# Performance work log

Measured on AMD Instinct MI355X. Metric: run time of the kernel, lower is better.

Reference implementation:

```python
import jax, jax.numpy as jnp
import numpy as np
import math

B, N, D, H = 4, 1024, 256, 8  # batch, points, dim_V, heads
DH = D // H                   # per-head dim = 32
INF = jnp.float32(1e38)


def setup_inputs() -> dict:
    key = jax.random.key(0)
    ks = jax.random.split(key, 16)
    s = 0.02
    inp = {
        "X_lift": jax.random.normal(ks[0], (B, N, 3), jnp.float32),
        "Y_lift": jax.random.normal(ks[1], (B, N, D), jnp.float32),
        "X_pairs": jax.random.normal(ks[2], (B, N, N, 3), jnp.float32),
        "presence_q": (jax.random.uniform(ks[3], (B, N)) < 0.9).astype(jnp.float32),
        "presence_k": (jax.random.uniform(ks[4], (B, N)) < 0.9).astype(jnp.float32),
        # projection weights, stored [in, out]
        "Wq": jax.random.normal(ks[5], (D, D), jnp.float32) * s,
        "bq": jnp.zeros((D,), jnp.float32),
        "Wk": jax.random.normal(ks[6], (D, D), jnp.float32) * s,
        "bk": jnp.zeros((D,), jnp.float32),
        "Wv": jax.random.normal(ks[7], (D, D), jnp.float32) * s,
        "bv": jnp.zeros((D,), jnp.float32),
        "Wo": jax.random.normal(ks[8], (D, D), jnp.float32) * s,
        "bo": jnp.zeros((D,), jnp.float32),
        # per-head location-bias MLPs: Linear(3,3) -> ReLU -> Linear(3,1)
        "Wg1": jax.random.normal(ks[9], (H, 3, 3), jnp.float32) * 0.5,
        "bg1": jnp.zeros((H, 3), jnp.float32),
        "wg2": jax.random.normal(ks[10], (H, 3), jnp.float32) * 0.5,
        "bg2": jnp.zeros((H,), jnp.float32),
    }
    return inp


def reference(X_lift, Y_lift, X_pairs, presence_q, presence_k,
              Wq, bq, Wk, bk, Wv, bv, Wo, bo, Wg1, bg1, wg2, bg2):
    # X_lift is unused by the original forward (keys=queries=values=Y_lift)
    Q = Y_lift @ Wq + bq          # [B,N,D]
    K = Y_lift @ Wk + bk
    V = Y_lift @ Wv + bv

    # split into heads, head-major layout [H,B,N,DH]
    Qh = Q.reshape(B, N, H, DH).transpose(2, 0, 1, 3)
    Kh = K.reshape(B, N, H, DH).transpose(2, 0, 1, 3)
    Vh = V.reshape(B, N, H, DH).transpose(2, 0, 1, 3)

    content = jnp.einsum('hbnd,hbmd->hbnm', Qh, Kh) / math.sqrt(D)

    # per-head pairwise location bias MLP on X_pairs [B,N,N,3]
    hid = jax.nn.relu(jnp.einsum('bnmc,hcd->hbnmd', X_pairs, Wg1)
                      + bg1[:, None, None, None, :])       # [H,B,N,N,3]
    loc = jnp.einsum('hbnmd,hd->hbnm', hid, wg2) + bg2[:, None, None, None]

    logits = content + loc                                  # [H,B,N,N]

    pq = presence_q[None, :, :, None]                       # [1,B,N,1]
    logits = pq * logits - (1.0 - pq) * INF
    pk = presence_k[None, :, None, :]                       # [1,B,1,N]
    logits = pk * logits - (1.0 - pk) * INF

    A = jax.nn.softmax(logits, axis=-1)                     # [H,B,N,N]
    Oh = jnp.einsum('hbnm,hbmd->hbnd', A, Vh)               # [H,B,N,DH]
    O = V + Oh.transpose(1, 2, 0, 3).reshape(B, N, D)       # residual on values
    O = O + jax.nn.relu(O @ Wo + bo)
    return O
```

## Files before the change

kernel.cpp:

```cpp
#include <hip/hip_runtime.h>
#include <hip/hip_bf16.h>
#include <math.h>

typedef __bf16 bf16;
typedef __bf16 bf16x4 __attribute__((ext_vector_type(4)));
typedef __bf16 bf16x8 __attribute__((ext_vector_type(8)));
typedef float f32x2 __attribute__((ext_vector_type(2)));
typedef float f32x4 __attribute__((ext_vector_type(4)));

#define NB 4
#define NN 1024
#define ND 256
#define NH 8
#define INFV 1e38f
#define RTHR2 11.5f
#define LOG2E 1.44269504f
#define ZSPLIT 4

__device__ __forceinline__ f32x4 mfma16(bf16x8 a, bf16x8 b, f32x4 c) {
    return __builtin_amdgcn_mfma_f32_16x16x32_bf16(a, b, c, 0, 0, 0);
}
__device__ __forceinline__ f32x2 sp2(float v) { return f32x2{v, v}; }
__device__ __forceinline__ f32x2 fma2(f32x2 a, float b, f32x2 c) {
    return __builtin_elementwise_fma(a, sp2(b), c);
}
__device__ __forceinline__ unsigned cvtpk(float lo, float hi) {
    unsigned r;
    asm("v_cvt_pk_bf16_f32 %0, %1, %2" : "=v"(r) : "v"(lo), "v"(hi));
    return r;
}

template<int MODE>
__global__ __launch_bounds__(256)
void gemm_k(const float* __restrict__ A,
            const float* __restrict__ W0, const float* __restrict__ b0,
            const float* __restrict__ W1, const float* __restrict__ b1,
            const float* __restrict__ W2, const float* __restrict__ b2,
            float* __restrict__ Fo2, bf16* __restrict__ G0,
            bf16* __restrict__ G1, bf16* __restrict__ Gt,
            float* __restrict__ Fo1, const float* __restrict__ addsrc)
{
    const int z = blockIdx.z;
    const float* W    = (z == 0) ? W0 : (z == 1) ? W1 : W2;
    const float* bias = (z == 0) ? b0 : (z == 1) ? b1 : b2;

    const int brow = blockIdx.x * 64;
    const int bcol = blockIdx.y * 64;
    const int t    = threadIdx.x;
    const int lane = t & 63;
    const int w    = t >> 6;
    const int wr   = w >> 1, wc = w & 1;
    const int g    = lane >> 4;
    const int l16  = lane & 15;

    __shared__ bf16 As[64][40];
    __shared__ bf16 Wt[64][40];

    f32x4 acc[2][2];
    #pragma unroll
    for (int i = 0; i < 2; ++i)
        #pragma unroll
        for (int j = 0; j < 2; ++j) acc[i][j] = f32x4{0.f, 0.f, 0.f, 0.f};

    const int ar = t >> 2, aj = (t & 3) * 8;
    const int wcid = t & 63, wk = (t >> 6) * 8;

    for (int k0 = 0; k0 < 256; k0 += 32) {
        {
            const float4 v0 = *(const float4*)&A[(size_t)(brow + ar)*ND + k0 + aj];
            const float4 v1 = *(const float4*)&A[(size_t)(brow + ar)*ND + k0 + aj + 4];
            bf16x8 w8 = { (bf16)v0.x, (bf16)v0.y, (bf16)v0.z, (bf16)v0.w,
                          (bf16)v1.x, (bf16)v1.y, (bf16)v1.z, (bf16)v1.w };
            *(bf16x8*)&As[ar][aj] = w8;
        }
        {
            bf16x8 w8;
            #pragma unroll
            for (int p = 0; p < 8; ++p)
                w8[p] = (bf16)W[(size_t)(k0 + wk + p)*ND + bcol + wcid];
            *(bf16x8*)&Wt[wcid][wk] = w8;
        }
        __syncthreads();

        bf16x8 af[2], bfj[2];
        #pragma unroll
        for (int i = 0; i < 2; ++i) af[i]  = *(const bf16x8*)&As[wr*32 + i*16 + l16][8*g];
        #pragma unroll
        for (int j = 0; j < 2; ++j) bfj[j] = *(const bf16x8*)&Wt[wc*32 + j*16 + l16][8*g];
        #pragma unroll
        for (int j = 0; j < 2; ++j)
            #pragma unroll
            for (int i = 0; i < 2; ++i) acc[i][j] = mfma16(af[i], bfj[j], acc[i][j]);
        __syncthreads();
    }

    #pragma unroll
    for (int j = 0; j < 2; ++j) {
        const int col = bcol + wc*32 + j*16 + l16;
        const float bj = bias[col];
        #pragma unroll
        for (int i = 0; i < 2; ++i) {
            const int row0 = brow + wr*32 + i*16 + 4*g;
            if (MODE == 1) {
                #pragma unroll
                for (int r = 0; r < 4; ++r) {
                    const size_t idx = (size_t)(row0 + r)*ND + col;
                    Fo1[idx] = addsrc[idx] + fmaxf(acc[i][j][r] + bj, 0.f);
                }
            } else if (z < 2) {
                bf16* Go = (z == 0) ? G0 : G1;
                #pragma unroll
                for (int r = 0; r < 4; ++r)
                    Go[(size_t)(row0 + r)*ND + col] = (bf16)(acc[i][j][r] + bj);
            } else {
                float vv[4];
                #pragma unroll
                for (int r = 0; r < 4; ++r) {
                    vv[r] = acc[i][j][r] + bj;
                    Fo2[(size_t)(row0 + r)*ND + col] = vv[r];
                }
                const int b2 = row0 >> 10;
                const int n0 = row0 & 1023;
                bf16x4 tv = { (bf16)vv[0], (bf16)vv[1], (bf16)vv[2], (bf16)vv[3] };
                *(bf16x4*)&Gt[((size_t)b2*ND + col)*NN + n0] = tv;
            }
        }
    }
}

__global__ __launch_bounds__(512, 4)
void attn_k(const bf16* __restrict__ Qb, const bf16* __restrict__ Kb,
            const bf16* __restrict__ Vt, const float* __restrict__ Xpg,
            const float* __restrict__ prq, const float* __restrict__ prk,
            const float* __restrict__ Wg1, const float* __restrict__ bg1,
            const float* __restrict__ wg2, const float* __restrict__ bg2,
            float* __restrict__ Ohp, float* __restrict__ ml)
{
    const int b    = blockIdx.y;
    const int q0   = blockIdx.x * 16;
    const int z    = blockIdx.z;
    const int mb0  = z * (NN/ZSPLIT);
    const int t    = threadIdx.x;
    const int w    = t >> 6;
    const int lane = t & 63;
    const int g    = lane >> 4;
    const int l16  = lane & 15;
    const int NT   = NN/ZSPLIT/32;

    __shared__ float Xps[2][16*132];

    float g1[3][3], gb1[3], g2v[3], gb2v;
    #pragma unroll
    for (int c = 0; c < 3; ++c)
        #pragma unroll
        for (int d = 0; d < 3; ++d) g1[c][d] = Wg1[(w*3 + c)*3 + d];
    #pragma unroll
    for (int d = 0; d < 3; ++d) { gb1[d] = bg1[w*3 + d]; g2v[d] = wg2[w*3 + d]*LOG2E; }
    gb2v = bg2[w]*LOG2E;
    const float sscale = 0.0625f * LOG2E;

    const bf16x8 qf = *(const bf16x8*)&Qb[((size_t)b*NN + q0 + l16)*ND + w*32 + 8*g];
    const bool okq = prq[b*NN + q0 + l16] > 0.5f;

    float m_run = -INFINITY, l_run = 0.f;
    f32x4 oh[2];
    oh[0] = f32x4{0.f,0.f,0.f,0.f};
    oh[1] = f32x4{0.f,0.f,0.f,0.f};

    const int aA = (((g & 1) * 2) * 16 + l16) * 4;
    const int aB = aA + 64;

    const bf16*  kp0 = &Kb[((size_t)b*NN + mb0 + l16)*ND + w*32 + 8*g];
    const bf16*  kp1 = kp0 + (size_t)16*ND;
    const bf16*  vp0 = &Vt[((size_t)b*ND + w*32 + l16)*NN + mb0 + 8*g];
    const bf16*  vp1 = vp0 + (size_t)16*NN;
    const int    xq  = t >> 5, xm = t & 31;
    const float* xpp = &Xpg[(((size_t)b*NN + q0 + xq)*NN + mb0 + xm)*3];
    const float* pkp = &prk[(size_t)b*NN + mb0];

    bf16x8 kf0 = *(const bf16x8*)kp0;
    bf16x8 kf1 = *(const bf16x8*)kp1;
    {
        float4 xv = { xpp[0], xpp[1], xpp[2], 0.f };
        *(float4*)&Xps[0][xq*132 + xm*4] = xv;
    }
    __syncthreads();

    #pragma unroll 2
    for (int it = 0; it < NT; ++it) {
        const int cur = it & 1;
        const int m0  = it * 32;

        const bf16x8 vf0 = *(const bf16x8*)(vp0 + m0);
        const bf16x8 vf1 = *(const bf16x8*)(vp1 + m0);
        const float4 pka = *(const float4*)&pkp[m0 + 4*g];
        const float4 pkb = *(const float4*)&pkp[m0 + 16 + 4*g];
        bf16x8 kn0, kn1;
        float  xnx = 0.f, xny = 0.f, xnz = 0.f;
        if (it + 1 < NT) {
            const int off = (it + 1) * 32;
            kn0 = *(const bf16x8*)(kp0 + (size_t)off*ND);
            kn1 = *(const bf16x8*)(kp1 + (size_t)off*ND);
            xnx = xpp[(size_t)off*3];
            xny = xpp[(size_t)off*3 + 1];
            xnz = xpp[(size_t)off*3 + 2];
        }

        const f32x4 zero = {0.f,0.f,0.f,0.f};
        f32x4 s[2];
        s[0] = mfma16(kf0, qf, zero);
        s[1] = mfma16(kf1, qf, zero);

        float lv[2][4];
        #pragma unroll
        for (int mg = 0; mg < 2; ++mg) {
            const float4 pk4 = mg ? pkb : pka;
            #pragma unroll
            for (int rp = 0; rp < 2; ++rp) {
                const int mA = mg*16 + 4*g + 2*rp;
                const float4 xa = *(const float4*)&Xps[cur][l16*132 + mA*4];
                const float4 xb = *(const float4*)&Xps[cur][l16*132 + (mA+1)*4];
                const f32x2 vx = {xa.x, xb.x};
                const f32x2 vy = {xa.y, xb.y};
                const f32x2 vz = {xa.z, xb.z};
                f32x2 h0 = fma2(vz, g1[2][0], fma2(vy, g1[1][0], fma2(vx, g1[0][0], sp2(gb1[0]))));
                f32x2 h1 = fma2(vz, g1[2][1], fma2(vy, g1[1][1], fma2(vx, g1[0][1], sp2(gb1[1]))));
                f32x2 h2 = fma2(vz, g1[2][2], fma2(vy, g1[1][2], fma2(vx, g1[0][2], sp2(gb1[2]))));
                const f32x2 zz = {0.f, 0.f};
                h0 = __builtin_elementwise_max(h0, zz);
                h1 = __builtin_elementwise_max(h1, zz);
                h2 = __builtin_elementwise_max(h2, zz);
                f32x2 loc = fma2(h2, g2v[2], fma2(h1, g2v[1], fma2(h0, g2v[0], sp2(gb2v))));
                const f32x2 s2 = { s[mg][2*rp], s[mg][2*rp+1] };
                const f32x2 y = fma2(s2, sscale, loc);
                lv[mg][2*rp]   = (okq && pk4[2*rp]   > 0.5f) ? y.x : -INFV;
                lv[mg][2*rp+1] = (okq && pk4[2*rp+1] > 0.5f) ? y.y : -INFV;
            }
        }

        float pm = fmaxf(fmaxf(fmaxf(lv[0][0], lv[0][1]), fmaxf(lv[0][2], lv[0][3])),
                         fmaxf(fmaxf(lv[1][0], lv[1][1]), fmaxf(lv[1][2], lv[1][3])));
        if (!__all((int)(pm <= m_run + RTHR2))) {
            float mx = pm;
            mx = fmaxf(mx, __shfl_xor(mx, 16));
            mx = fmaxf(mx, __shfl_xor(mx, 32));
            const float mnew = fmaxf(m_run, mx);
            const float corr = exp2f(m_run - mnew);
            l_run *= corr;
            #pragma unroll
            for (int r = 0; r < 4; ++r) { oh[0][r] *= corr; oh[1][r] *= corr; }
            m_run = mnew;
        }
        float pp0[4], pp1[4];
        #pragma unroll
        for (int r = 0; r < 4; ++r) {
            pp0[r] = exp2f(lv[0][r] - m_run);
            pp1[r] = exp2f(lv[1][r] - m_run);
        }
        l_run += (pp0[0] + pp0[1]) + (pp0[2] + pp0[3])
               + (pp1[0] + pp1[1]) + (pp1[2] + pp1[3]);

        const unsigned A0 = cvtpk(pp0[0], pp0[1]);
        const unsigned A1 = cvtpk(pp0[2], pp0[3]);
        const unsigned B0 = cvtpk(pp1[0], pp1[1]);
        const unsigned B1 = cvtpk(pp1[2], pp1[3]);
        const bool lo = (lane < 32);
        const int w0a = __builtin_amdgcn_ds_bpermute(aA, (int)A0);
        const int w0b = __builtin_amdgcn_ds_bpermute(aA, (int)B0);
        const int w1a = __builtin_amdgcn_ds_bpermute(aA, (int)A1);
        const int w1b = __builtin_amdgcn_ds_bpermute(aA, (int)B1);
        const int w2a = __builtin_amdgcn_ds_bpermute(aB, (int)A0);
        const int w2b = __builtin_amdgcn_ds_bpermute(aB, (int)B0);
        const int w3a = __builtin_amdgcn_ds_bpermute(aB, (int)A1);
        const int w3b = __builtin_amdgcn_ds_bpermute(aB, (int)B1);
        union { int i[4]; bf16x8 v; } pu;
        pu.i[0] = lo ? w0a : w0b;
        pu.i[1] = lo ? w1a : w1b;
        pu.i[2] = lo ? w2a : w2b;
        pu.i[3] = lo ? w3a : w3b;

        oh[0] = mfma16(vf0, pu.v, oh[0]);
        oh[1] = mfma16(vf1, pu.v, oh[1]);

        if (it + 1 < NT) {
            float4 xv = { xnx, xny, xnz, 0.f };
            *(float4*)&Xps[cur ^ 1][xq*132 + xm*4] = xv;
            kf0 = kn0; kf1 = kn1;
        }
        __syncthreads();
    }

    float ls = l_run;
    ls += __shfl_xor(ls, 16);
    ls += __shfl_xor(ls, 32);
    const int n = q0 + l16;
    const size_t obase = (((size_t)z*NB + b)*NN + n)*ND + w*32;
    *(f32x4*)&Ohp[obase + 4*g]      = oh[0];
    *(f32x4*)&Ohp[obase + 16 + 4*g] = oh[1];
    if (g == 0) {
        const size_t mi = ((((size_t)z*NB + b)*NN + n)*NH + w)*2;
        ml[mi]   = m_run;
        ml[mi+1] = ls;
    }
}

__global__ __launch_bounds__(256)
void comb_k(const float* __restrict__ Ohp, const float* __restrict__ ml,
            const float* __restrict__ Vf, float* __restrict__ O1)
{
    const int idx = blockIdx.x * 256 + threadIdx.x;
    const int dq = idx & 63;
    const int bn = idx >> 6;
    const int d0 = dq * 4;
    const int h  = dq >> 3;

    const size_t base = ((size_t)bn*NH + h)*2;
    const size_t zstr = (size_t)NB*NN*NH*2;
    float mz[ZSPLIT], lz[ZSPLIT];
    float M = -INFINITY;
    #pragma unroll
    for (int zi = 0; zi < ZSPLIT; ++zi) {
        mz[zi] = ml[base + zi*zstr];
        lz[zi] = ml[base + zi*zstr + 1];
        M = fmaxf(M, mz[zi]);
    }
    float wz[ZSPLIT], den = 0.f;
    #pragma unroll
    for (int zi = 0; zi < ZSPLIT; ++zi) {
        wz[zi] = exp2f(mz[zi] - M);
        den = fmaf(lz[zi], wz[zi], den);
    }
    const float inv = 1.f / den;

    const size_t e = (size_t)bn*ND + d0;
    f32x4 num = {0.f,0.f,0.f,0.f};
    #pragma unroll
    for (int zi = 0; zi < ZSPLIT; ++zi) {
        const f32x4 o = *(const f32x4*)&Ohp[e + (size_t)zi*NB*NN*ND];
        #pragma unroll
        for (int r = 0; r < 4; ++r) num[r] = fmaf(o[r], wz[zi], num[r]);
    }
    const f32x4 vf = *(const f32x4*)&Vf[e];
    f32x4 out;
    #pragma unroll
    for (int r = 0; r < 4; ++r) out[r] = vf[r] + num[r]*inv;
    *(f32x4*)&O1[e] = out;
}

extern "C" void kernel_launch(void* const* d_in, const int* in_sizes, int n_in,
                              void* d_out, int out_size, void* d_ws, size_t ws_size,
                              hipStream_t stream)
{
    const float* Y   = (const float*)d_in[1];
    const float* Xp  = (const float*)d_in[2];
    const float* prq = (const float*)d_in[3];
    const float* prk = (const float*)d_in[4];
    const float* Wq  = (const float*)d_in[5];
    const float* bq  = (const float*)d_in[6];
    const float* Wk  = (const float*)d_in[7];
    const float* bk  = (const float*)d_in[8];
    const float* Wv  = (const float*)d_in[9];
    const float* bv  = (const float*)d_in[10];
    const float* Wo  = (const float*)d_in[11];
    const float* bo  = (const float*)d_in[12];
    const float* Wg1 = (const float*)d_in[13];
    const float* bg1 = (const float*)d_in[14];
    const float* wg2 = (const float*)d_in[15];
    const float* bg2 = (const float*)d_in[16];
    float* out = (float*)d_out;

    const size_t BND = (size_t)NB * NN * ND;
    float* Vf  = (float*)d_ws;
    float* Ohp = Vf + BND;
    float* ml  = Ohp + (size_t)ZSPLIT*BND;
    bf16*  Qb  = (bf16*)(ml + (size_t)ZSPLIT*NB*NN*NH*2);
    bf16*  Kb  = Qb + BND;
    bf16*  Vt  = Kb + BND;
    float* O1  = (float*)Qb;

    gemm_k<0><<<dim3(64, 4, 3), 256, 0, stream>>>(
        Y, Wq, bq, Wk, bk, Wv, bv,
        Vf, Qb, Kb, Vt, nullptr, nullptr);

    attn_k<<<dim3(NN/16, NB, ZSPLIT), 512, 0, stream>>>(
        Qb, Kb, Vt, Xp, prq, prk, Wg1, bg1, wg2, bg2, Ohp, ml);

    comb_k<<<dim3(1024), 256, 0, stream>>>(Ohp, ml, Vf, O1);

    gemm_k<1><<<dim3(64, 4, 1), 256, 0, stream>>>(
        O1, Wo, bo, Wo, bo, Wo, bo,
        nullptr, nullptr, nullptr, nullptr, out, O1);
}
```

Before: 77.29 us.

## Load X_pairs directly into registers per lane, drop LDS staging and barriers

Removes the shared-memory double buffer for X_pairs and the per-iteration __syncthreads. Each lane now reads its own 4 consecutive key positions (12 floats) as three float4 global loads that match the MFMA output layout. Software prefetch of K and X_pairs is also dropped, and the loop is no longer unrolled. The aim is to cut LDS traffic and block-level synchronisation. The cost is that all eight waves now load the same X_pairs data redundantly from global/L2 memory, and the lost prefetch exposes load latency.

Result: slower. 111.1 us (+43.7%).

```diff
diff --git a/kernel.cpp b/kernel.cpp
--- a/kernel.cpp
+++ b/kernel.cpp
@@ -147,8 +147,6 @@
     const int l16  = lane & 15;
     const int NT   = NN/ZSPLIT/32;
 
-    __shared__ float Xps[2][16*132];
-
     float g1[3][3], gb1[3], g2v[3], gb2v;
     #pragma unroll
     for (int c = 0; c < 3; ++c)
@@ -174,37 +172,27 @@
     const bf16*  kp1 = kp0 + (size_t)16*ND;
     const bf16*  vp0 = &Vt[((size_t)b*ND + w*32 + l16)*NN + mb0 + 8*g];
     const bf16*  vp1 = vp0 + (size_t)16*NN;
-    const int    xq  = t >> 5, xm = t & 31;
-    const float* xpp = &Xpg[(((size_t)b*NN + q0 + xq)*NN + mb0 + xm)*3];
+    const float* xpl = &Xpg[(((size_t)b*NN + q0 + l16)*NN + mb0)*3];
     const float* pkp = &prk[(size_t)b*NN + mb0];
 
-    bf16x8 kf0 = *(const bf16x8*)kp0;
-    bf16x8 kf1 = *(const bf16x8*)kp1;
-    {
-        float4 xv = { xpp[0], xpp[1], xpp[2], 0.f };
-        *(float4*)&Xps[0][xq*132 + xm*4] = xv;
-    }
-    __syncthreads();
-
-    #pragma unroll 2
+    #pragma unroll 1
     for (int it = 0; it < NT; ++it) {
-        const int cur = it & 1;
-        const int m0  = it * 32;
-
+        const int m0 = it * 32;
+
+        const bf16x8 kf0 = *(const bf16x8*)(kp0 + (size_t)m0*ND);
+        const bf16x8 kf1 = *(const bf16x8*)(kp1 + (size_t)m0*ND);
         const bf16x8 vf0 = *(const bf16x8*)(vp0 + m0);
         const bf16x8 vf1 = *(const bf16x8*)(vp1 + m0);
         const float4 pka = *(const float4*)&pkp[m0 + 4*g];
         const float4 pkb = *(const float4*)&pkp[m0 + 16 + 4*g];
-        bf16x8 kn0, kn1;
-        float  xnx = 0.f, xny = 0.f, xnz = 0.f;
-        if (it + 1 < NT) {
-            const int off = (it + 1) * 32;
-            kn0 = *(const bf16x8*)(kp0 + (size_t)off*ND);
-            kn1 = *(const bf16x8*)(kp1 + (size_t)off*ND);
-            xnx = xpp[(size_t)off*3];
-            xny = xpp[(size_t)off*3 + 1];
-            xnz = xpp[(size_t)off*3 + 2];
-        }
+        const float* xc = xpl + (size_t)(m0 + 4*g)*3;
+        const float4 c0 = *(const float4*)(xc);
+        const float4 c1 = *(const float4*)(xc + 4);
+        const float4 c2 = *(const float4*)(xc + 8);
+        const float* xd = xpl + (size_t)(m0 + 16 + 4*g)*3;
+        const float4 d0 = *(const float4*)(xd);
+        const float4 d1 = *(const float4*)(xd + 4);
+        const float4 d2 = *(const float4*)(xd + 8);
 
         const f32x4 zero = {0.f,0.f,0.f,0.f};
         f32x4 s[2];
@@ -215,14 +203,14 @@
         #pragma unroll
         for (int mg = 0; mg < 2; ++mg) {
             const float4 pk4 = mg ? pkb : pka;
+            const float4 e0 = mg ? d0 : c0;
+            const float4 e1 = mg ? d1 : c1;
+            const float4 e2 = mg ? d2 : c2;
             #pragma unroll
             for (int rp = 0; rp < 2; ++rp) {
-                const int mA = mg*16 + 4*g + 2*rp;
-                const float4 xa = *(const float4*)&Xps[cur][l16*132 + mA*4];
-                const float4 xb = *(const float4*)&Xps[cur][l16*132 + (mA+1)*4];
-                const f32x2 vx = {xa.x, xb.x};
-                const f32x2 vy = {xa.y, xb.y};
-                const f32x2 vz = {xa.z, xb.z};
+                f32x2 vx, vy, vz;
+                if (rp == 0) { vx = f32x2{e0.x, e0.w}; vy = f32x2{e0.y, e1.x}; vz = f32x2{e0.z, e1.y}; }
+                else         { vx = f32x2{e1.z, e2.y}; vy = f32x2{e1.w, e2.z}; vz = f32x2{e2.x, e2.w}; }
                 f32x2 h0 = fma2(vz, g1[2][0], fma2(vy, g1[1][0], fma2(vx, g1[0][0], sp2(gb1[0]))));
                 f32x2 h1 = fma2(vz, g1[2][1], fma2(vy, g1[1][1], fma2(vx, g1[0][1], sp2(gb1[1]))));
                 f32x2 h2 = fma2(vz, g1[2][2], fma2(vy, g1[1][2], fma2(vx, g1[0][2], sp2(gb1[2]))));
@@ -281,13 +269,6 @@
 
         oh[0] = mfma16(vf0, pu.v, oh[0]);
         oh[1] = mfma16(vf1, pu.v, oh[1]);
-
-        if (it + 1 < NT) {
-            float4 xv = { xnx, xny, xnz, 0.f };
-            *(float4*)&Xps[cur ^ 1][xq*132 + xm*4] = xv;
-            kf0 = kn0; kf1 = kn1;
-        }
-        __syncthreads();
     }
 
     float ls = l_run;
```
